# Kernel optimization log

Hardware: AMD Instinct MI355X
Metric: run time of the kernel (lower is better)

## Reference

```python
import jax, jax.numpy as jnp
import numpy as np
from jax import lax

B, S, D_IN = 4, 4096, 1024
D_FAST, D_SLOW = 512, 512
Z_BIAS_FAST, Z_BIAS_SLOW = 2.0, -2.0


def _binop(q_i, q_j):
    a_i, b_i = q_i
    a_j, b_j = q_j
    return (a_i * a_j, a_j * b_i + b_j)


def parallel_scan(a, b):
    # h_t = a_t * h_{t-1} + b_t along seq axis (axis=1)
    _, h = lax.associative_scan(_binop, (a, b), axis=1)
    return h


def setup_inputs() -> dict:
    key = jax.random.key(0)
    ks = jax.random.split(key, 6)
    scale = 0.02
    x = jax.random.normal(ks[0], (B, S, D_IN), dtype=jnp.float32)
    W_zf = jax.random.normal(ks[1], (D_IN, D_FAST), dtype=jnp.float32) * scale
    b_zf = jnp.full((D_FAST,), Z_BIAS_FAST, dtype=jnp.float32)
    W_hf = jax.random.normal(ks[2], (D_IN, D_FAST), dtype=jnp.float32) * scale
    b_hf = jnp.zeros((D_FAST,), dtype=jnp.float32)
    W_zs = jax.random.normal(ks[3], (D_IN, D_SLOW), dtype=jnp.float32) * scale
    b_zs = jnp.full((D_SLOW,), Z_BIAS_SLOW, dtype=jnp.float32)
    W_hs = jax.random.normal(ks[4], (D_IN, D_SLOW), dtype=jnp.float32) * scale
    b_hs = jnp.zeros((D_SLOW,), dtype=jnp.float32)
    W_g = jax.random.normal(ks[5], (D_FAST + D_SLOW, D_FAST + D_SLOW), dtype=jnp.float32) * scale
    b_g = jnp.zeros((D_FAST + D_SLOW,), dtype=jnp.float32)
    return {"x": x, "W_zf": W_zf, "b_zf": b_zf, "W_hf": W_hf, "b_hf": b_hf,
            "W_zs": W_zs, "b_zs": b_zs, "W_hs": W_hs, "b_hs": b_hs,
            "W_g": W_g, "b_g": b_g}


def reference(x, W_zf, b_zf, W_hf, b_hf, W_zs, b_zs, W_hs, b_hs, W_g, b_g):
    # Fast compartment (coupling='output' => slow branch sees raw x)
    z_fast = jax.nn.sigmoid(jnp.einsum('bsd,df->bsf', x, W_zf) + b_zf)
    h_tilde_fast = jnp.einsum('bsd,df->bsf', x, W_hf) + b_hf
    h_fast = parallel_scan(1.0 - z_fast, z_fast * h_tilde_fast)

    # Slow compartment
    z_slow = jax.nn.sigmoid(jnp.einsum('bsd,df->bsf', x, W_zs) + b_zs)
    h_tilde_slow = jnp.einsum('bsd,df->bsf', x, W_hs) + b_hs
    h_slow = parallel_scan(1.0 - z_slow, z_slow * h_tilde_slow)

    h_combined = jnp.concatenate([h_fast, h_slow], axis=-1)  # (B, S, D_FAST+D_SLOW)
    gate = jax.nn.sigmoid(jnp.einsum('bsc,cd->bsd', h_combined, W_g) + b_g)
    return gate * h_combined
```

## Files before the change

kernel.cpp:

```cpp
#include <hip/hip_runtime.h>

#define BB 4
#define SS 4096
#define DIN 1024
#define DH 1024
#define PN 2048
#define MM (BB*SS)
#define NC 64
#define CL 64

typedef unsigned short ushort_t;
typedef __attribute__((ext_vector_type(8))) short bf16x8;
typedef __attribute__((ext_vector_type(4))) float f32x4;
typedef __attribute__((ext_vector_type(4))) unsigned short u16x4;

__device__ inline float bf2f(ushort_t u) {
    union { float f; unsigned int i; } v; v.i = ((unsigned int)u) << 16; return v.f;
}
__device__ inline ushort_t f2bf(float f) {
    union { float f; unsigned int i; } v; v.f = f;
    unsigned int r = v.i + 0x7fffu + ((v.i >> 16) & 1u);
    return (ushort_t)(r >> 16);
}
__device__ inline float sigmoidf_(float x) { return 1.0f / (1.0f + __expf(-x)); }

__device__ inline void load_lds16(const void* g, void* l) {
    __builtin_amdgcn_global_load_lds(
        (const __attribute__((address_space(1))) void*)g,
        (__attribute__((address_space(3))) void*)l, 16, 0, 0);
}

__device__ __forceinline__ bf16x8 ds128(const ushort_t* p) {
    bf16x8 r;
    asm volatile("ds_read_b128 %0, %1"
                 : "=v"(r)
                 : "v"((const __attribute__((address_space(3))) ushort_t*)p));
    return r;
}

__global__ void zero_out_kernel(float* out, int n) {
    int i = blockIdx.x * 256 + threadIdx.x;
    if (i < n) out[i] = 0.0f;
}

#define PREP_NBLK 17160
__global__ __launch_bounds__(256) void prep_kernel(
    const float* __restrict__ x,
    const float* __restrict__ Wzf, const float* __restrict__ Wzs,
    const float* __restrict__ Whf, const float* __restrict__ Whs,
    const float* __restrict__ Wg,
    const float* __restrict__ bzf, const float* __restrict__ bzs,
    const float* __restrict__ bhf, const float* __restrict__ bhs,
    ushort_t* __restrict__ WcatT, ushort_t* __restrict__ WgT,
    ushort_t* __restrict__ Xb, float* __restrict__ bcat)
{
    __shared__ ushort_t tile[64][65];
    const int bx = blockIdx.x, tid = threadIdx.x;

    if (bx < 768) {
        const float* src; ushort_t* dst; int srcN, t;
        if (bx < 512) {
            int wi = bx >> 7; t = bx & 127; srcN = 512;
            const float* S[4] = {Wzf, Wzs, Whf, Whs};
            src = S[wi];
            dst = WcatT + (size_t)(wi * 512) * DIN;
        } else {
            t = bx - 512; srcN = 1024; src = Wg; dst = WgT;
        }
        const int k0 = (t & 15) * 64, n0 = (t >> 4) * 64;
        const int tx = tid & 63, ty = tid >> 6;
        #pragma unroll
        for (int i = ty; i < 64; i += 4)
            tile[i][tx] = f2bf(src[(size_t)(k0 + i) * srcN + n0 + tx]);
        __syncthreads();
        #pragma unroll
        for (int i = ty; i < 64; i += 4)
            dst[(size_t)(n0 + i) * DIN + k0 + tx] = tile[tx][i];
    } else if (bx < 17152) {
        size_t i = ((size_t)(bx - 768) * 256 + tid) * 4;
        float4 v = *(const float4*)(x + i);
        u16x4 o;
        o.x = f2bf(v.x); o.y = f2bf(v.y); o.z = f2bf(v.z); o.w = f2bf(v.w);
        *(u16x4*)(Xb + i) = o;
    } else {
        int i = (bx - 17152) * 256 + tid;
        float v = (i < 512) ? bzf[i] : (i < 1024) ? bzs[i - 512]
                : (i < 1536) ? bhf[i - 1024] : bhs[i - 1536];
        bcat[i] = v;
    }
}

#define BARR __builtin_amdgcn_s_barrier()
#define WAITK { asm volatile("s_waitcnt lgkmcnt(0)"); __builtin_amdgcn_sched_barrier(0); }
#define VM4   { asm volatile("s_waitcnt vmcnt(4)");   __builtin_amdgcn_sched_barrier(0); }

#define STG_A(b, h, kt) { \
    _Pragma("unroll") \
    for (int j = 0; j < 2; j++) { \
        int c = wave * 2 + j; \
        load_lds16(Ablk + (size_t)((h) * 128 + c * 8) * lda + (kt) * 64 + laneAOff, \
                   &As[(b) * 16384 + (h) * 8192 + c * 512]); \
    } }

#define STG_B(b, h, kt) { \
    _Pragma("unroll") \
    for (int j = 0; j < 2; j++) { \
        int c = wave * 2 + j; \
        load_lds16(Bblk + (size_t)((h) * 128 + c * 8) * K + (kt) * 64 + laneBOff, \
                   &Bs[(b) * 16384 + (h) * 8192 + c * 512]); \
    } }

#define LOADA(b, qm) { \
    const ushort_t* p0 = &As[(b) * 16384 + (qm) * 8192 + arow0 + acol0]; \
    const ushort_t* p1 = &As[(b) * 16384 + (qm) * 8192 + arow0 + acol1]; \
    _Pragma("unroll") \
    for (int mt = 0; mt < 4; mt++) { \
        af[mt][0] = ds128(p0 + mt * 1024); \
        af[mt][1] = ds128(p1 + mt * 1024); \
    } }

#define LOADB(b, qn, bq) { \
    const ushort_t* p0 = &Bs[(b) * 16384 + (qn) * 8192 + brow0 + acol0]; \
    const ushort_t* p1 = &Bs[(b) * 16384 + (qn) * 8192 + brow0 + acol1]; \
    _Pragma("unroll") \
    for (int nt = 0; nt < 2; nt++) { \
        bq[nt][0] = ds128(p0 + nt * 1024); \
        bq[nt][1] = ds128(p1 + nt * 1024); \
    } }

#define MFMA16(qm, qn, bq) { \
    __builtin_amdgcn_s_setprio(1); \
    _Pragma("unroll") \
    for (int kh = 0; kh < 2; kh++) { \
        _Pragma("unroll") \
        for (int mt = 0; mt < 4; mt++) { \
            _Pragma("unroll") \
            for (int nt = 0; nt < 2; nt++) { \
                acc[qm][qn][mt][nt] = __builtin_amdgcn_mfma_f32_16x16x32_bf16( \
                    af[mt][kh], bq[nt][kh], acc[qm][qn][mt][nt], 0, 0, 0); \
            } } } \
    __builtin_amdgcn_s_setprio(0); }

template <int EPI, int NB>
__global__ __launch_bounds__(512, 2) void gemm_kernel(
    const ushort_t* __restrict__ A, const ushort_t* __restrict__ Bt,
    int K, int lda,
    const float* __restrict__ bias,
    ushort_t* __restrict__ Zarr, ushort_t* __restrict__ Harr,
    const float* __restrict__ bg, const ushort_t* __restrict__ Hbf,
    float* __restrict__ Out)
{
    __shared__ alignas(16) ushort_t As[2 * 256 * 64];
    __shared__ alignas(16) ushort_t Bs[2 * 256 * 64];

    const int tid  = threadIdx.x;
    const int lane = tid & 63;
    const int wave = tid >> 6;
    const int wm   = wave & 1;
    const int wn   = wave >> 1;
    const int lrow = lane & 15;
    const int kgrp = lane >> 4;

    const int id  = blockIdx.x;
    const int xcd = id & 7;
    const int s   = id >> 3;
    const int mBase = (xcd + 8 * (s / NB)) * 256;
    const int nBase = (s % NB) * 256;

    f32x4 acc[2][2][4][2] = {};

    const ushort_t* Ablk = A  + (size_t)mBase * lda;
    const ushort_t* Bblk = Bt + (size_t)nBase * K;
    const int laneAOff = (lane >> 3) * lda + (((lane & 7) ^ (lane >> 3)) * 8);
    const int laneBOff = (lane >> 3) * K   + (((lane & 7) ^ (lane >> 3)) * 8);

    const int arow0 = (wm * 64 + lrow) * 64;
    const int brow0 = (wn * 32 + lrow) * 64;
    const int acol0 = ((kgrp    ) ^ (lrow & 7)) * 8;
    const int acol1 = ((4 + kgrp) ^ (lrow & 7)) * 8;

    const int NKT = K >> 6;
    const int NIT = NKT >> 1;

    bf16x8 af[4][2], bqA[2][2], bqB[2][2];

    STG_A(0, 0, 0); STG_B(0, 0, 0); STG_A(0, 1, 0); STG_B(0, 1, 0);
    STG_A(1, 0, 1); STG_B(1, 0, 1);
    VM4;
    BARR;

    for (int i = 0; i < NIT; i++) {
        const int kt1  = 2 * i + 1;
        const int ktn0 = (2 * i + 2) & (NKT - 1);
        const int ktn1 = (2 * i + 3) & (NKT - 1);

        LOADA(0, 0); LOADB(0, 0, bqA); STG_A(1, 1, kt1);
        BARR; WAITK; MFMA16(0, 0, bqA); BARR;
        LOADB(0, 1, bqB); STG_B(1, 1, kt1);
        BARR; WAITK; MFMA16(0, 1, bqB); BARR;
        LOADA(0, 1); STG_A(0, 0, ktn0);
        BARR; WAITK; MFMA16(1, 1, bqB); BARR;
        STG_B(0, 0, ktn0);
        BARR; MFMA16(1, 0, bqA); VM4; BARR;

        LOADA(1, 0); LOADB(1, 0, bqA); STG_B(0, 1, ktn0);
        BARR; WAITK; MFMA16(0, 0, bqA); BARR;
        LOADB(1, 1, bqB); STG_A(0, 1, ktn0);
        BARR; WAITK; MFMA16(0, 1, bqB); BARR;
        LOADA(1, 1); STG_A(1, 0, ktn1);
        BARR; WAITK; MFMA16(1, 1, bqB); BARR;
        STG_B(1, 0, ktn1);
        BARR; MFMA16(1, 0, bqA); VM4; BARR;
    }
    WAITK;

    const int rquad = (lane >> 4) * 4;

    if (EPI == 0) {
        const bool isz = (nBase < DH);
        ushort_t* Dst  = isz ? Zarr : Harr;
        const int csub = isz ? 0 : DH;
        #pragma unroll
        for (int qm = 0; qm < 2; qm++)
        #pragma unroll
        for (int qn = 0; qn < 2; qn++)
        #pragma unroll
        for (int nt = 0; nt < 2; nt++) {
            int col  = nBase + qn * 128 + wn * 32 + nt * 16 + lrow;
            float bv = bias[col];
            int dcol = col - csub;
            #pragma unroll
            for (int mt = 0; mt < 4; mt++) {
                int row = mBase + qm * 128 + wm * 64 + mt * 16 + rquad;
                ushort_t* p = Dst + (size_t)row * DH + dcol;
                #pragma unroll
                for (int r = 0; r < 4; r++) {
                    float v = acc[qm][qn][mt][nt][r] + bv;
                    if (isz) v = sigmoidf_(v);
                    p[(size_t)r * DH] = f2bf(v);
                }
            }
        }
    } else {
        #pragma unroll
        for (int qm = 0; qm < 2; qm++)
        #pragma unroll
        for (int qn = 0; qn < 2; qn++)
        #pragma unroll
        for (int nt = 0; nt < 2; nt++) {
            int col  = nBase + qn * 128 + wn * 32 + nt * 16 + lrow;
            float bv = bg[col];
            #pragma unroll
            for (int mt = 0; mt < 4; mt++) {
                int row = mBase + qm * 128 + wm * 64 + mt * 16 + rquad;
                #pragma unroll
                for (int r = 0; r < 4; r++) {
                    float g = sigmoidf_(acc[qm][qn][mt][nt][r] + bv);
                    float h = bf2f(Hbf[(size_t)(row + r) * DH + col]);
                    Out[(size_t)(row + r) * DH + col] = g * h;
                }
            }
        }
    }
}

__global__ __launch_bounds__(256) void scan_chunk_agg(
    const ushort_t* __restrict__ Zarr, const ushort_t* __restrict__ Harr,
    float* __restrict__ Agg, float* __restrict__ Bagg)
{
    const int c4    = threadIdx.x * 4;
    const int chunk = blockIdx.x;
    const int b     = blockIdx.y;
    const size_t s0 = ((size_t)b * SS + (size_t)chunk * CL) * DH + c4;
    const ushort_t* Zp = Zarr + s0;
    const ushort_t* Hp = Harr + s0;

    float A0 = 1.0f, A1 = 1.0f, A2 = 1.0f, A3 = 1.0f;
    float B0 = 0.0f, B1 = 0.0f, B2 = 0.0f, B3 = 0.0f;
    #pragma unroll 8
    for (int t = 0; t < CL; t++) {
        u16x4 zv = *(const u16x4*)(Zp + (size_t)t * DH);
        u16x4 hv = *(const u16x4*)(Hp + (size_t)t * DH);
        float z0 = bf2f(zv.x), z1 = bf2f(zv.y), z2 = bf2f(zv.z), z3 = bf2f(zv.w);
        float h0 = bf2f(hv.x), h1 = bf2f(hv.y), h2 = bf2f(hv.z), h3 = bf2f(hv.w);
        A0 *= 1.0f - z0;  B0 = (1.0f - z0) * B0 + z0 * h0;
        A1 *= 1.0f - z1;  B1 = (1.0f - z1) * B1 + z1 * h1;
        A2 *= 1.0f - z2;  B2 = (1.0f - z2) * B2 + z2 * h2;
        A3 *= 1.0f - z3;  B3 = (1.0f - z3) * B3 + z3 * h3;
    }
    const size_t idx = ((size_t)(b * NC + chunk)) * DH + c4;
    *(float4*)(Agg  + idx) = make_float4(A0, A1, A2, A3);
    *(float4*)(Bagg + idx) = make_float4(B0, B1, B2, B3);
}

__global__ void scan_carry(const float* __restrict__ Agg, const float* __restrict__ Bagg,
                           float* __restrict__ Hinit)
{
    const int i = blockIdx.x * 256 + threadIdx.x;
    const int b = i >> 10, c = i & 1023;
    float h = 0.0f;
    for (int j = 0; j < NC; j++) {
        const size_t idx = ((size_t)(b * NC + j)) * DH + c;
        Hinit[idx] = h;
        h = Agg[idx] * h + Bagg[idx];
    }
}

__global__ __launch_bounds__(256) void scan_apply(
    const ushort_t* __restrict__ Zarr, ushort_t* Harr, const float* __restrict__ Hinit)
{
    const int c4    = threadIdx.x * 4;
    const int chunk = blockIdx.x;
    const int b     = blockIdx.y;
    const size_t s0 = ((size_t)b * SS + (size_t)chunk * CL) * DH + c4;
    const ushort_t* Zp = Zarr + s0;
    ushort_t*       Hp = Harr + s0;

    float4 hi = *(const float4*)(Hinit + ((size_t)(b * NC + chunk)) * DH + c4);
    float h0 = hi.x, h1 = hi.y, h2 = hi.z, h3 = hi.w;
    #pragma unroll 8
    for (int t = 0; t < CL; t++) {
        u16x4 zv = *(const u16x4*)(Zp + (size_t)t * DH);
        u16x4 hv = *(const u16x4*)(Hp + (size_t)t * DH);
        float z0 = bf2f(zv.x), z1 = bf2f(zv.y), z2 = bf2f(zv.z), z3 = bf2f(zv.w);
        float t0 = bf2f(hv.x), t1 = bf2f(hv.y), t2 = bf2f(hv.z), t3 = bf2f(hv.w);
        h0 = (1.0f - z0) * h0 + z0 * t0;
        h1 = (1.0f - z1) * h1 + z1 * t1;
        h2 = (1.0f - z2) * h2 + z2 * t2;
        h3 = (1.0f - z3) * h3 + z3 * t3;
        u16x4 o;
        o.x = f2bf(h0); o.y = f2bf(h1); o.z = f2bf(h2); o.w = f2bf(h3);
        *(u16x4*)(Hp + (size_t)t * DH) = o;
    }
}

extern "C" void kernel_launch(void* const* d_in, const int* in_sizes, int n_in,
                              void* d_out, int out_size, void* d_ws, size_t ws_size,
                              hipStream_t stream)
{
    const float* x   = (const float*)d_in[0];
    const float* Wzf = (const float*)d_in[1];
    const float* bzf = (const float*)d_in[2];
    const float* Whf = (const float*)d_in[3];
    const float* bhf = (const float*)d_in[4];
    const float* Wzs = (const float*)d_in[5];
    const float* bzs = (const float*)d_in[6];
    const float* Whs = (const float*)d_in[7];
    const float* bhs = (const float*)d_in[8];
    const float* Wg  = (const float*)d_in[9];
    const float* bg  = (const float*)d_in[10];

    const size_t NEED = (size_t)42 << 20;
    if (ws_size < NEED) {
        zero_out_kernel<<<(MM * DH + 255) / 256, 256, 0, stream>>>((float*)d_out, MM * DH);
        return;
    }

    char* ws = (char*)d_ws;
    ushort_t* WcatT = (ushort_t*)(ws);
    ushort_t* WgT   = (ushort_t*)(ws + ((size_t)4 << 20));
    float*    bcat  = (float*)   (ws + ((size_t)6 << 20));
    float*    Agg   = (float*)   (ws + ((size_t)6 << 20) + (64 << 10));
    float*    Bagg  = (float*)   (ws + ((size_t)7 << 20) + (64 << 10));
    float*    Hinit = (float*)   (ws + ((size_t)8 << 20) + (64 << 10));
    ushort_t* Harr  = (ushort_t*)(ws + ((size_t)10 << 20));

    ushort_t* Xb   = (ushort_t*)d_out;
    ushort_t* Zarr = Xb + (size_t)MM * DH;

    dim3 blk(256);

    prep_kernel<<<PREP_NBLK, blk, 0, stream>>>(
        x, Wzf, Wzs, Whf, Whs, Wg, bzf, bzs, bhf, bhs, WcatT, WgT, Xb, bcat);

    gemm_kernel<0, PN / 256><<<(MM / 256) * (PN / 256), dim3(512), 0, stream>>>(
        Xb, WcatT, DIN, DIN, bcat, Zarr, Harr, nullptr, nullptr, nullptr);

    scan_chunk_agg<<<dim3(NC, BB), blk, 0, stream>>>(Zarr, Harr, Agg, Bagg);
    scan_carry<<<16, 256, 0, stream>>>(Agg, Bagg, Hinit);
    scan_apply<<<dim3(NC, BB), blk, 0, stream>>>(Zarr, Harr, Hinit);

    gemm_kernel<1, DH / 256><<<(MM / 256) * (DH / 256), dim3(512), 0, stream>>>(
        Harr, WgT, DIN, DH, nullptr, nullptr, nullptr, bg, Harr,
        (float*)d_out);
}
```

Before: 308.5 us.

## Software-pipeline LDS fragment loads into MFMA blocks with register rotation

Restructures the GEMM main loop so LDS-to-register fragment loads for the next quadrant are interleaved with the MFMA instructions of the current quadrant, rotating A and B fragment registers as each k-half finishes. The prologue stages two full k-tiles and preloads the first fragments, and each step has one barrier instead of two around its MFMA block. The aim is to hide ds_read latency behind matrix-core work and cut barrier stalls. It relies on a delicate hazard ordering between global-to-LDS staging and fragment reads across buffers, which carries correctness and register-pressure risk.

```diff
diff --git a/kernel.cpp b/kernel.cpp
--- a/kernel.cpp
+++ b/kernel.cpp
@@ -91,8 +91,10 @@
 }
 
 #define BARR __builtin_amdgcn_s_barrier()
-#define WAITK { asm volatile("s_waitcnt lgkmcnt(0)"); __builtin_amdgcn_sched_barrier(0); }
-#define VM4   { asm volatile("s_waitcnt vmcnt(4)");   __builtin_amdgcn_sched_barrier(0); }
+#define SB0  __builtin_amdgcn_sched_barrier(0)
+#define WAITK { asm volatile("s_waitcnt lgkmcnt(0)"); SB0; }
+#define VM4   { asm volatile("s_waitcnt vmcnt(4)");   SB0; }
+#define VM8   { asm volatile("s_waitcnt vmcnt(8)");   SB0; }
 
 #define STG_A(b, h, kt) { \
     _Pragma("unroll") \
@@ -110,36 +112,66 @@
                    &Bs[(b) * 16384 + (h) * 8192 + c * 512]); \
     } }
 
-#define LOADA(b, qm) { \
-    const ushort_t* p0 = &As[(b) * 16384 + (qm) * 8192 + arow0 + acol0]; \
-    const ushort_t* p1 = &As[(b) * 16384 + (qm) * 8192 + arow0 + acol1]; \
+#define KHBLK(qm, qn, bq, kh) { \
     _Pragma("unroll") \
     for (int mt = 0; mt < 4; mt++) { \
-        af[mt][0] = ds128(p0 + mt * 1024); \
-        af[mt][1] = ds128(p1 + mt * 1024); \
-    } }
-
-#define LOADB(b, qn, bq) { \
-    const ushort_t* p0 = &Bs[(b) * 16384 + (qn) * 8192 + brow0 + acol0]; \
-    const ushort_t* p1 = &Bs[(b) * 16384 + (qn) * 8192 + brow0 + acol1]; \
+        _Pragma("unroll") \
+        for (int nt = 0; nt < 2; nt++) { \
+            acc[qm][qn][mt][nt] = __builtin_amdgcn_mfma_f32_16x16x32_bf16( \
+                af[mt][kh], bq[nt][kh], acc[qm][qn][mt][nt], 0, 0, 0); \
+        } } }
+
+#define AROT(qm, qn, bq, b, h) { \
+    const ushort_t* pa0 = &As[(b) * 16384 + (h) * 8192 + arow0 + acol0]; \
+    const ushort_t* pa1 = &As[(b) * 16384 + (h) * 8192 + arow0 + acol1]; \
+    _Pragma("unroll") \
+    for (int mt = 0; mt < 4; mt++) { \
+        acc[qm][qn][mt][0] = __builtin_amdgcn_mfma_f32_16x16x32_bf16( \
+            af[mt][1], bq[0][1], acc[qm][qn][mt][0], 0, 0, 0); \
+        acc[qm][qn][mt][1] = __builtin_amdgcn_mfma_f32_16x16x32_bf16( \
+            af[mt][1], bq[1][1], acc[qm][qn][mt][1], 0, 0, 0); \
+        SB0; \
+        af[mt][0] = ds128(pa0 + mt * 1024); \
+        af[mt][1] = ds128(pa1 + mt * 1024); \
+        SB0; \
+    } }
+
+#define BROT(qm, qn, bq, b, h) { \
+    const ushort_t* pb0 = &Bs[(b) * 16384 + (h) * 8192 + brow0 + acol0]; \
+    const ushort_t* pb1 = &Bs[(b) * 16384 + (h) * 8192 + brow0 + acol1]; \
     _Pragma("unroll") \
     for (int nt = 0; nt < 2; nt++) { \
-        bq[nt][0] = ds128(p0 + nt * 1024); \
-        bq[nt][1] = ds128(p1 + nt * 1024); \
-    } }
-
-#define MFMA16(qm, qn, bq) { \
-    __builtin_amdgcn_s_setprio(1); \
-    _Pragma("unroll") \
-    for (int kh = 0; kh < 2; kh++) { \
         _Pragma("unroll") \
         for (int mt = 0; mt < 4; mt++) { \
-            _Pragma("unroll") \
-            for (int nt = 0; nt < 2; nt++) { \
-                acc[qm][qn][mt][nt] = __builtin_amdgcn_mfma_f32_16x16x32_bf16( \
-                    af[mt][kh], bq[nt][kh], acc[qm][qn][mt][nt], 0, 0, 0); \
-            } } } \
-    __builtin_amdgcn_s_setprio(0); }
+            acc[qm][qn][mt][nt] = __builtin_amdgcn_mfma_f32_16x16x32_bf16( \
+                af[mt][1], bq[nt][1], acc[qm][qn][mt][nt], 0, 0, 0); \
+        } \
+        SB0; \
+        bq[nt][0] = ds128(pb0 + nt * 1024); \
+        bq[nt][1] = ds128(pb1 + nt * 1024); \
+        SB0; \
+    } }
+
+#define LOADBQ(bq, b, h) { \
+    const ushort_t* pb0 = &Bs[(b) * 16384 + (h) * 8192 + brow0 + acol0]; \
+    const ushort_t* pb1 = &Bs[(b) * 16384 + (h) * 8192 + brow0 + acol1]; \
+    _Pragma("unroll") \
+    for (int nt = 0; nt < 2; nt++) { \
+        bq[nt][0] = ds128(pb0 + nt * 1024); \
+        bq[nt][1] = ds128(pb1 + nt * 1024); \
+    } }
+
+#define LOADAF(b, h) { \
+    const ushort_t* pa0 = &As[(b) * 16384 + (h) * 8192 + arow0 + acol0]; \
+    const ushort_t* pa1 = &As[(b) * 16384 + (h) * 8192 + arow0 + acol1]; \
+    _Pragma("unroll") \
+    for (int mt = 0; mt < 4; mt++) { \
+        af[mt][0] = ds128(pa0 + mt * 1024); \
+        af[mt][1] = ds128(pa1 + mt * 1024); \
+    } }
+
+#define PRIO1 __builtin_amdgcn_s_setprio(1)
+#define PRIO0 __builtin_amdgcn_s_setprio(0)
 
 template <int EPI, int NB>
 __global__ __launch_bounds__(512, 2) void gemm_kernel(
@@ -182,35 +214,78 @@
     const int NKT = K >> 6;
     const int NIT = NKT >> 1;
 
-    bf16x8 af[4][2], bqA[2][2], bqB[2][2];
-
-    STG_A(0, 0, 0); STG_B(0, 0, 0); STG_A(0, 1, 0); STG_B(0, 1, 0);
-    STG_A(1, 0, 1); STG_B(1, 0, 1);
-    VM4;
+    bf16x8 af[4][2], bqX[2][2], bqY[2][2];
+
+    STG_B(0, 0, 0); STG_A(0, 0, 0); STG_B(0, 1, 0); STG_A(0, 1, 0);
+    STG_B(1, 0, 1); STG_A(1, 0, 1); STG_B(1, 1, 1); STG_A(1, 1, 1);
+    VM8;
     BARR;
+    LOADBQ(bqX, 0, 0);
+    LOADAF(0, 0);
 
     for (int i = 0; i < NIT; i++) {
-        const int kt1  = 2 * i + 1;
         const int ktn0 = (2 * i + 2) & (NKT - 1);
         const int ktn1 = (2 * i + 3) & (NKT - 1);
 
-        LOADA(0, 0); LOADB(0, 0, bqA); STG_A(1, 1, kt1);
-        BARR; WAITK; MFMA16(0, 0, bqA); BARR;
-        LOADB(0, 1, bqB); STG_B(1, 1, kt1);
-        BARR; WAITK; MFMA16(0, 1, bqB); BARR;
-        LOADA(0, 1); STG_A(0, 0, ktn0);
-        BARR; WAITK; MFMA16(1, 1, bqB); BARR;
+        WAITK; BARR;
         STG_B(0, 0, ktn0);
-        BARR; MFMA16(1, 0, bqA); VM4; BARR;
-
-        LOADA(1, 0); LOADB(1, 0, bqA); STG_B(0, 1, ktn0);
-        BARR; WAITK; MFMA16(0, 0, bqA); BARR;
-        LOADB(1, 1, bqB); STG_A(0, 1, ktn0);
-        BARR; WAITK; MFMA16(0, 1, bqB); BARR;
-        LOADA(1, 1); STG_A(1, 0, ktn1);
-        BARR; WAITK; MFMA16(1, 1, bqB); BARR;
+        PRIO1;
+        KHBLK(0, 0, bqX, 0);
+        SB0; LOADBQ(bqY, 0, 1); SB0;
+        KHBLK(0, 0, bqX, 1);
+        PRIO0;
+
+        WAITK; BARR;
+        STG_A(0, 0, ktn0);
+        PRIO1;
+        KHBLK(0, 1, bqY, 0);
+        AROT(0, 1, bqY, 0, 1);
+        PRIO0;
+        VM4;
+
+        WAITK; BARR;
+        STG_B(0, 1, ktn0);
+        PRIO1;
+        KHBLK(1, 1, bqY, 0);
+        BROT(1, 1, bqY, 1, 0);
+        PRIO0;
+
+        WAITK; BARR;
+        STG_A(0, 1, ktn0);
+        PRIO1;
+        KHBLK(1, 0, bqX, 0);
+        AROT(1, 0, bqX, 1, 0);
+        PRIO0;
+
+        WAITK; BARR;
         STG_B(1, 0, ktn1);
-        BARR; MFMA16(1, 0, bqA); VM4; BARR;
+        PRIO1;
+        KHBLK(0, 0, bqY, 0);
+        SB0; LOADBQ(bqX, 1, 1); SB0;
+        KHBLK(0, 0, bqY, 1);
+        PRIO0;
+
+        WAITK; BARR;
+        STG_A(1, 0, ktn1);
+        PRIO1;
+        KHBLK(0, 1, bqX, 0);
+        AROT(0, 1, bqX, 1, 1);
+        PRIO0;
+        VM4;
+
+        WAITK; BARR;
+        STG_B(1, 1, ktn1);
+        PRIO1;
+        KHBLK(1, 1, bqX, 0);
+        BROT(1, 1, bqX, 0, 0);
+        PRIO0;
+
+        WAITK; BARR;
+        STG_A(1, 1, ktn1);
+        PRIO1;
+        KHBLK(1, 0, bqY, 0);
+        AROT(1, 0, bqY, 0, 0);
+        PRIO0;
     }
     WAITK;
 
```

Result: slower. 545.0 us (+76.6%).
